# Performance work log

Measured on AMD Instinct MI355X. Metric: run time of the kernel, lower is better.

The kernel has to match this reference:

```python
import jax, jax.numpy as jnp
import numpy as np

WIN = 7          # window width (matches init win_size)
EPS = 1e-4       # Tikhonov regularization for the per-pixel normal equations
NF = 8           # features: [1, depth, albedo(3), normal(3)]


def _box_sum(x, win):
    # (windows are clipped at image borders, as in the CUDA kernel).
    ndim = x.ndim
    wdims = (1,) * (ndim - 2) + (win, win)
    return jax.lax.reduce_window(x, 0.0, jax.lax.add, wdims, (1,) * ndim, 'SAME')


def setup_inputs() -> dict:
    key = jax.random.key(0)
    k1, k2, k3, k4 = jax.random.split(key, 4)
    B, H, W = 1, 1024, 1024
    inp = jax.random.normal(k1, (B, 3, H, W), dtype=jnp.float32)
    depth = jax.random.uniform(k2, (B, 1, H, W), dtype=jnp.float32)
    albedo = jax.random.uniform(k3, (B, 3, H, W), dtype=jnp.float32)
    normal = jax.random.normal(k4, (B, 3, H, W), dtype=jnp.float32)
    normal = normal / (jnp.linalg.norm(normal, axis=1, keepdims=True) + 1e-6)
    return {"input": inp, "depth": depth, "albedo": albedo, "normal": normal}


def reference(input, depth, albedo, normal):
    B, C, H, W = input.shape
    ones = jnp.ones((B, 1, H, W), dtype=input.dtype)
    # Feature maps f: [B, 8, H, W] = [1, depth, albedo, normal]
    f = jnp.concatenate([ones, depth, albedo, normal], axis=1)

    # Per-pixel normal equations via box-filtered feature products.
    # AtA[b,i,j,h,w] = sum_{window} f_i * f_j   -> [B, 8, 8, H, W]
    AtA = _box_sum(f[:, :, None] * f[:, None], WIN)
    # AtY[b,i,c,h,w] = sum_{window} f_i * y_c   -> [B, 8, 3, H, W]
    AtY = _box_sum(f[:, :, None] * input[:, None], WIN)

    AtA = jnp.moveaxis(AtA, (1, 2), (3, 4))  # [B, H, W, 8, 8]
    AtY = jnp.moveaxis(AtY, (1, 2), (3, 4))  # [B, H, W, 8, 3]
    AtA = AtA + EPS * jnp.eye(NF, dtype=input.dtype)

    # Batched 8x8 solves, one per pixel.
    beta = jnp.linalg.solve(AtA, AtY)  # [B, H, W, 8, 3]

    # Evaluate fitted model at the center pixel's features.
    out = jnp.einsum('bhwfc,bfhw->bchw', beta, f)
    return out
```

## Files before the change

kernel.cpp:

```cpp
#include <hip/hip_runtime.h>
#include <math.h>

#define HH 1024
#define WW 1024
#define OUTW 58
#define RPB 4
#define WPB 4
#define OFF(i) ((i)*8 - (i)*((i)-1)/2)


template<int CTRL>
__device__ __forceinline__ float dpp0(float x) {
    return __int_as_float(
        __builtin_amdgcn_update_dpp(0, __float_as_int(x), CTRL, 0xf, 0xf, true));
}
__device__ __forceinline__ float wshr1(float x) { return dpp0<0x138>(x); }

__device__ __forceinline__ float frcp_fast(float s) {
    float r = __builtin_amdgcn_rcpf(s);
    return r * fmaf(-s, r, 2.0f);
}

__global__ __launch_bounds__(WPB * 64, 2) void ls_sep_kernel(
    const float* __restrict__ inp,
    const float* __restrict__ dep,
    const float* __restrict__ alb,
    const float* __restrict__ nrm,
    float* __restrict__ out)
{
    const int L  = threadIdx.x & 63;
    const int wv = threadIdx.x >> 6;
    const int HW = HH * WW;
    const int x  = OUTW * blockIdx.x - 3 + L;
    const int y0 = (RPB * WPB) * blockIdx.y + RPB * wv;
    const int px = x - 3;

    const int xc    = min(max(x, 0), WW - 1);
    const float xok = (x >= 0 && x < WW) ? 1.f : 0.f;

    float C[60];
    #pragma unroll
    for (int k = 0; k < 60; k++) C[k] = 0.f;

    auto acc_row = [&](int yy, float sgn) {
        const int yc = min(max(yy, 0), HH - 1);
        const float ok = (yy >= 0 && yy < HH) ? xok : 0.f;
        const int p = yc * WW + xc;
        float fv[8], yv[3];
        fv[0] = 1.f;
        fv[1] = dep[p];
        fv[2] = alb[p];
        fv[3] = alb[p + HW];
        fv[4] = alb[p + 2 * HW];
        fv[5] = nrm[p];
        fv[6] = nrm[p + HW];
        fv[7] = nrm[p + 2 * HW];
        yv[0] = inp[p];
        yv[1] = inp[p + HW];
        yv[2] = inp[p + 2 * HW];
        const float s = sgn * ok;
        float fs[8];
        #pragma unroll
        for (int i = 0; i < 8; i++) fs[i] = fv[i] * s;
        int k = 0;
        #pragma unroll
        for (int i = 0; i < 8; i++)
            #pragma unroll
            for (int j = i; j < 8; j++) { C[k] = fmaf(fs[i], fv[j], C[k]); k++; }
        #pragma unroll
        for (int i = 0; i < 8; i++)
            #pragma unroll
            for (int c = 0; c < 3; c++)
                C[36 + i * 3 + c] = fmaf(fs[i], yv[c], C[36 + i * 3 + c]);
    };

    #pragma unroll 1
    for (int yy = y0 - 4; yy < y0 + 3; yy++) acc_row(yy, 1.f);

    const int idxm4 = ((L - 4) & 63) << 2;
    const int pxc = min(max(px, 0), WW - 1);
    const bool do_store = (L >= 6) && (px < WW);

    auto htap12 = [&](int base, float* dst) {
        float t2a[12];
        int pma[12];
        #pragma unroll
        for (int j = 0; j < 12; j++) {
            const float xv = C[base + j];
            const float w1 = wshr1(xv);
            const float t1 = xv + w1;
            const float w2 = wshr1(w1);
            const float t3 = t1 + w2;
            const float w3 = wshr1(w2);
            t2a[j] = t3 + w3;
            pma[j] = __builtin_amdgcn_ds_bpermute(idxm4, __float_as_int(t3));
        }
        #pragma unroll
        for (int j = 0; j < 12; j++)
            dst[j] = t2a[j] + __int_as_float(pma[j]);
    };

    #pragma unroll 1
    for (int y = y0; y < y0 + RPB; y++) {
        acc_row(y + 3, 1.f);
        acc_row(y - 4, -1.f);

        const int pc = y * WW + pxc;
        float cf[8];
        cf[0] = 1.f;
        cf[1] = dep[pc];
        cf[2] = alb[pc]; cf[3] = alb[pc + HW]; cf[4] = alb[pc + 2 * HW];
        cf[5] = nrm[pc]; cf[6] = nrm[pc + HW]; cf[7] = nrm[pc + 2 * HW];

        float W[36];
        htap12(0,  &W[0]);
        htap12(12, &W[12]);
        htap12(24, &W[24]);
        #pragma unroll
        for (int i = 0; i < 8; i++) W[OFF(i)] += 1.0e-4f;

        float idv[8];
        #pragma unroll
        for (int i = 0; i < 8; i++) {
            #pragma unroll
            for (int k = 0; k < i; k++) {
                const float c = W[OFF(k) + i - k] * idv[k];
                #pragma unroll
                for (int j = i; j < 8; j++)
                    W[OFF(i) + j - i] = fmaf(-c, W[OFF(k) + j - k], W[OFF(i) + j - i]);
            }
            idv[i] = frcp_fast(W[OFF(i)]);
        }

        float vt[8];
        #pragma unroll
        for (int i = 0; i < 8; i++) {
            float s = cf[i];
            #pragma unroll
            for (int k = 0; k < i; k++)
                s = fmaf(-W[OFF(k) + i - k], vt[k], s);
            vt[i] = s * idv[i];
        }
        float w[8];
        #pragma unroll
        for (int i = 7; i >= 0; i--) {
            float t = 0.f;
            #pragma unroll
            for (int j = i + 1; j < 8; j++)
                t = fmaf(W[OFF(i) + j - i], w[j], t);
            w[i] = fmaf(-idv[i], t, vt[i]);
        }

        float r[3] = {0.f, 0.f, 0.f};
        {
            float SY[12];
            htap12(36, SY);
            #pragma unroll
            for (int i = 0; i < 4; i++)
                #pragma unroll
                for (int c = 0; c < 3; c++)
                    r[c] = fmaf(w[i], SY[i * 3 + c], r[c]);
            htap12(48, SY);
            #pragma unroll
            for (int i = 0; i < 4; i++)
                #pragma unroll
                for (int c = 0; c < 3; c++)
                    r[c] = fmaf(w[i + 4], SY[i * 3 + c], r[c]);
        }

        if (do_store) {
            const int p = y * WW + px;
            #pragma unroll
            for (int c = 0; c < 3; c++)
                out[c * HW + p] = r[c];
        }
    }
}

extern "C" void kernel_launch(void* const* d_in, const int* in_sizes, int n_in,
                              void* d_out, int out_size, void* d_ws, size_t ws_size,
                              hipStream_t stream) {
    const float* inp = (const float*)d_in[0];
    const float* dep = (const float*)d_in[1];
    const float* alb = (const float*)d_in[2];
    const float* nrm = (const float*)d_in[3];
    float* out = (float*)d_out;
    dim3 grid((WW + OUTW - 1) / OUTW, HH / (RPB * WPB));
    ls_sep_kernel<<<grid, dim3(WPB * 64), 0, stream>>>(inp, dep, alb, nrm, out);
}
```

Before: 126.8 us.

## Prefetch entering rows into LDS ring buffer via global_load_lds

```diff
diff --git a/kernel.cpp b/kernel.cpp
--- a/kernel.cpp
+++ b/kernel.cpp
@@ -6,6 +6,7 @@
 #define OUTW 58
 #define RPB 4
 #define WPB 4
+#define NF10 10
 #define OFF(i) ((i)*8 - (i)*((i)-1)/2)
 
 
@@ -20,6 +21,9 @@
     float r = __builtin_amdgcn_rcpf(s);
     return r * fmaf(-s, r, 2.0f);
 }
+
+typedef const __attribute__((address_space(1))) unsigned int* gptr_t;
+typedef __attribute__((address_space(3))) unsigned int* lptr_t;
 
 __global__ __launch_bounds__(WPB * 64, 2) void ls_sep_kernel(
     const float* __restrict__ inp,
@@ -28,54 +32,96 @@
     const float* __restrict__ nrm,
     float* __restrict__ out)
 {
+    __shared__ float ring[WPB][2][NF10][64];
+
     const int L  = threadIdx.x & 63;
     const int wv = threadIdx.x >> 6;
     const int HW = HH * WW;
-    const int x  = OUTW * blockIdx.x - 3 + L;
+    const int x0 = OUTW * blockIdx.x - 3;
+    const int x  = x0 + L;
     const int y0 = (RPB * WPB) * blockIdx.y + RPB * wv;
     const int px = x - 3;
 
     const int xc    = min(max(x, 0), WW - 1);
     const float xok = (x >= 0 && x < WW) ? 1.f : 0.f;
+    const bool edgeBlk = (blockIdx.x == 0) || (blockIdx.x == gridDim.x - 1);
 
     float C[60];
     #pragma unroll
     for (int k = 0; k < 60; k++) C[k] = 0.f;
 
-    auto acc_row = [&](int yy, float sgn) {
+    auto acc_vals = [&](const float fv7[7], const float yv[3], float s) {
+        float f8[8];
+        f8[0] = 1.f;
+        #pragma unroll
+        for (int i = 0; i < 7; i++) f8[i + 1] = fv7[i];
+        float fs[8];
+        #pragma unroll
+        for (int i = 0; i < 8; i++) fs[i] = f8[i] * s;
+        int k = 0;
+        #pragma unroll
+        for (int i = 0; i < 8; i++)
+            #pragma unroll
+            for (int j = i; j < 8; j++) { C[k] = fmaf(fs[i], f8[j], C[k]); k++; }
+        #pragma unroll
+        for (int i = 0; i < 8; i++)
+            #pragma unroll
+            for (int c = 0; c < 3; c++)
+                C[36 + i * 3 + c] = fmaf(fs[i], yv[c], C[36 + i * 3 + c]);
+    };
+
+    auto acc_row_g = [&](int yy, float sgn) {
         const int yc = min(max(yy, 0), HH - 1);
         const float ok = (yy >= 0 && yy < HH) ? xok : 0.f;
         const int p = yc * WW + xc;
-        float fv[8], yv[3];
-        fv[0] = 1.f;
-        fv[1] = dep[p];
-        fv[2] = alb[p];
-        fv[3] = alb[p + HW];
-        fv[4] = alb[p + 2 * HW];
-        fv[5] = nrm[p];
-        fv[6] = nrm[p + HW];
-        fv[7] = nrm[p + 2 * HW];
-        yv[0] = inp[p];
-        yv[1] = inp[p + HW];
-        yv[2] = inp[p + 2 * HW];
-        const float s = sgn * ok;
-        float fs[8];
-        #pragma unroll
-        for (int i = 0; i < 8; i++) fs[i] = fv[i] * s;
-        int k = 0;
-        #pragma unroll
-        for (int i = 0; i < 8; i++)
-            #pragma unroll
-            for (int j = i; j < 8; j++) { C[k] = fmaf(fs[i], fv[j], C[k]); k++; }
-        #pragma unroll
-        for (int i = 0; i < 8; i++)
-            #pragma unroll
-            for (int c = 0; c < 3; c++)
-                C[36 + i * 3 + c] = fmaf(fs[i], yv[c], C[36 + i * 3 + c]);
+        float fv7[7], yv[3];
+        fv7[0] = dep[p];
+        fv7[1] = alb[p]; fv7[2] = alb[p + HW]; fv7[3] = alb[p + 2 * HW];
+        fv7[4] = nrm[p]; fv7[5] = nrm[p + HW]; fv7[6] = nrm[p + 2 * HW];
+        yv[0] = inp[p]; yv[1] = inp[p + HW]; yv[2] = inp[p + 2 * HW];
+        acc_vals(fv7, yv, sgn * ok);
+    };
+
+    auto prefetch_row = [&](int yy, int slot) {
+        const int yc = min(max(yy, 0), HH - 1);
+        if (!edgeBlk) {
+            const float* bp[NF10] = {
+                dep + yc * WW + x0,
+                alb + yc * WW + x0, alb + HW + yc * WW + x0, alb + 2 * HW + yc * WW + x0,
+                nrm + yc * WW + x0, nrm + HW + yc * WW + x0, nrm + 2 * HW + yc * WW + x0,
+                inp + yc * WW + x0, inp + HW + yc * WW + x0, inp + 2 * HW + yc * WW + x0};
+            #pragma unroll
+            for (int f = 0; f < NF10; f++)
+                __builtin_amdgcn_global_load_lds(
+                    (gptr_t)(bp[f] + L), (lptr_t)&ring[wv][slot][f][0], 4, 0, 0);
+        } else {
+            const int p = yc * WW + xc;
+            ring[wv][slot][0][L] = dep[p];
+            ring[wv][slot][1][L] = alb[p];
+            ring[wv][slot][2][L] = alb[p + HW];
+            ring[wv][slot][3][L] = alb[p + 2 * HW];
+            ring[wv][slot][4][L] = nrm[p];
+            ring[wv][slot][5][L] = nrm[p + HW];
+            ring[wv][slot][6][L] = nrm[p + 2 * HW];
+            ring[wv][slot][7][L] = inp[p];
+            ring[wv][slot][8][L] = inp[p + HW];
+            ring[wv][slot][9][L] = inp[p + 2 * HW];
+        }
+    };
+
+    auto acc_enter_lds = [&](int yy, int slot) {
+        const float ok = (yy >= 0 && yy < HH) ? xok : 0.f;
+        float fv7[7], yv[3];
+        #pragma unroll
+        for (int i = 0; i < 7; i++) fv7[i] = ring[wv][slot][i][L];
+        #pragma unroll
+        for (int c = 0; c < 3; c++) yv[c] = ring[wv][slot][7 + c][L];
+        acc_vals(fv7, yv, ok);
     };
 
     #pragma unroll 1
-    for (int yy = y0 - 4; yy < y0 + 3; yy++) acc_row(yy, 1.f);
+    for (int yy = y0 - 4; yy < y0 + 3; yy++) acc_row_g(yy, 1.f);
+    prefetch_row(y0 + 3, (y0 + 3) & 1);
 
     const int idxm4 = ((L - 4) & 63) << 2;
     const int pxc = min(max(px, 0), WW - 1);
@@ -102,8 +148,12 @@
 
     #pragma unroll 1
     for (int y = y0; y < y0 + RPB; y++) {
-        acc_row(y + 3, 1.f);
-        acc_row(y - 4, -1.f);
+        __builtin_amdgcn_s_waitcnt(0x0f70);
+        asm volatile("" ::: "memory");
+        prefetch_row(y + 4, (y + 4) & 1);
+
+        acc_enter_lds(y + 3, (y + 3) & 1);
+        acc_row_g(y - 4, -1.f);
 
         const int pc = y * WW + pxc;
         float cf[8];
```

Result: slower. 156.7 us (+23.6%).
